# Kernel tuning notes

Measured on AMD Instinct MI355X. Metric: run time of the kernel, lower is better.

## Reference

```python
import jax, jax.numpy as jnp
import numpy as np
from jax import lax

W = 65536  # wavelength batch
L = 64     # number of stacked layers
N_IN = 1.0
N_OUT = 1.45
PURITY = 0.87
CD_SCALE = 32980.0  # mdeg conversion, as in source
LN10 = 2.302585092994046


def setup_inputs() -> dict:
    key = jax.random.key(0)
    ks = jax.random.split(key, 9)
    wl = jnp.linspace(0.4, 0.8, W, dtype=jnp.float32)  # microns, matches wl_range*1e-6 usage
    thickP = jax.random.normal(ks[0], (L,), jnp.float32) * 2.0

    def u(k, lo, hi):
        return lo + (hi - lo) * jax.random.uniform(k, (W, L), jnp.float32)

    return {
        "wl": wl,
        "thickP": thickP,
        "mind": jnp.float32(20.0),   # nm
        "maxd": jnp.float32(300.0),  # nm
        "eps_c_re": u(ks[1], 1.8, 4.5),
        "eps_c_im": u(ks[2], 0.0, 0.08),
        "kappa_c_re": u(ks[3], -5e-3, 5e-3),
        "kappa_c_im": u(ks[4], -5e-3, 5e-3),
        "eps_a_re": u(ks[5], 1.8, 4.5),
        "eps_a_im": u(ks[6], 0.0, 0.08),
        "kappa_a_re": u(ks[7], -5e-3, 5e-3),
        "kappa_a_im": u(ks[8], -5e-3, 5e-3),
    }


def _chain(Ms):
    # Ms: [L, W, 2, 2] complex; sequential layer chain-multiply (TMM recursion)
    eye = jnp.broadcast_to(jnp.eye(2, dtype=Ms.dtype), (Ms.shape[1], 2, 2))

    def step(carry, Ml):
        return jnp.einsum('wij,wjk->wik', carry, Ml), None

    Mt, _ = lax.scan(step, eye, Ms)
    return Mt  # [W, 2, 2]


def _absorbance(eps, kappa, sigma, k0, d):
    # Circular eigenmode TMM for Pasteur (isotropic chiral) layers at normal incidence.
    # eps, kappa: [W, L] complex relative quantities; k0: [W]; d: [L] meters.
    n0 = jnp.sqrt(eps)                       # background index, also wave admittance
    n_sig = n0 + sigma * kappa               # circular eigenmode index n +/- kappa
    delta = k0[:, None] * n_sig * d[None, :]  # [W, L] phase thickness
    c = jnp.cos(delta)
    s = jnp.sin(delta)
    Y = n0
    # characteristic matrix per layer: [[cos d, i sin d / Y], [i Y sin d, cos d]]
    M = jnp.stack([jnp.stack([c, 1j * s / Y], axis=-1),
                   jnp.stack([1j * Y * s, c], axis=-1)], axis=-2)  # [W, L, 2, 2]
    Mt = _chain(jnp.transpose(M, (1, 0, 2, 3)))
    m00, m01 = Mt[:, 0, 0], Mt[:, 0, 1]
    m10, m11 = Mt[:, 1, 0], Mt[:, 1, 1]
    denom = N_IN * (m00 + m01 * N_OUT) + (m10 + m11 * N_OUT)
    t = 2.0 * N_IN / denom
    T = (N_OUT / N_IN) * (jnp.abs(t) ** 2)
    return -jnp.log(T + 1e-12) / LN10  # absorbance per handedness


def _stack_cd_abs(eps_re, eps_im, kap_re, kap_im, k0, d):
    eps = (eps_re + 1j * eps_im).astype(jnp.complex64)
    kap = (kap_re + 1j * kap_im).astype(jnp.complex64)
    A_r = _absorbance(eps, kap, +1.0, k0, d)  # RCP
    A_l = _absorbance(eps, kap, -1.0, k0, d)  # LCP
    return A_l - A_r, 0.5 * (A_l + A_r)


def reference(wl, thickP, mind, maxd, eps_c_re, eps_c_im, kappa_c_re, kappa_c_im,
              eps_a_re, eps_a_im, kappa_a_re, kappa_a_im):
    d = (jax.nn.sigmoid(thickP) * (maxd - mind) + mind) * 1e-9  # [L] meters
    k0 = (2.0 * np.float32(3.1415926)) / (wl * 1e-6)             # [W]
    cd_c, abs_c = _stack_cd_abs(eps_c_re, eps_c_im, kappa_c_re, kappa_c_im, k0, d)
    cd_a, abs_a = _stack_cd_abs(eps_a_re, eps_a_im, kappa_a_re, kappa_a_im, k0, d)
    scale = (2.0 * PURITY - 1.0) * CD_SCALE
    return (cd_c * scale, cd_a * scale, abs_c, abs_a)
```

## Files before the change

kernel.cpp:

```cpp
#include <hip/hip_runtime.h>
#include <math.h>

#define LTOT 64
#define GL   4
#define LPL  (LTOT / GL)

#define INV2PI  0.15915494309189535f
#define LOG2E   1.4426950408889634f
#define LOG10_2 0.30102999566398120f

struct cpx { float r, i; };
struct Mat { cpx e00, e01, e10, e11; };

__device__ __forceinline__ cpx cmul(cpx a, cpx b) {
    return { fmaf(a.r, b.r, -a.i * b.i), fmaf(a.r, b.i, a.i * b.r) };
}
__device__ __forceinline__ cpx cmadd(cpx a, cpx b, cpx c) {
    return { fmaf(a.r, b.r, fmaf(-a.i, b.i, c.r)),
             fmaf(a.r, b.i, fmaf( a.i, b.r, c.i)) };
}
__device__ __forceinline__ Mat mmul(const Mat& A, const Mat& B) {
    Mat C;
    C.e00 = cmadd(A.e01, B.e10, cmul(A.e00, B.e00));
    C.e01 = cmadd(A.e01, B.e11, cmul(A.e00, B.e01));
    C.e10 = cmadd(A.e11, B.e10, cmul(A.e10, B.e00));
    C.e11 = cmadd(A.e11, B.e11, cmul(A.e10, B.e01));
    return C;
}
__device__ __forceinline__ cpx csqrt_pos(cpx z) {
    float m  = __builtin_amdgcn_sqrtf(fmaf(z.r, z.r, z.i * z.i));
    float re = __builtin_amdgcn_sqrtf(0.5f * (m + z.r));
    float im = 0.5f * z.i * __builtin_amdgcn_rcpf(re);
    return { re, im };
}

__device__ __forceinline__ void accum(Mat& P, bool first, float xrev, float y,
                                      cpx n0, float inv_n0sq) {
    float rf = __builtin_amdgcn_fractf(xrev);
    float s_ = __builtin_amdgcn_sinf(rf);
    float c_ = __builtin_amdgcn_cosf(rf);
    float y2 = y * y;
    float chv = fmaf(y2, fmaf(y2, 0.0416666667f, 0.5f), 1.0f);
    float shv = y * fmaf(y2, fmaf(y2, 0.0083333333f, 0.1666666667f), 1.0f);
    cpx cc = { c_ * chv, -s_ * shv };
    cpx ss = { s_ * chv,  c_ * shv };
    cpx qq = { (ss.r * n0.r + ss.i * n0.i) * inv_n0sq,
               (ss.i * n0.r - ss.r * n0.i) * inv_n0sq };
    cpx m01 = { -qq.i, qq.r };
    cpx p   = cmul(n0, ss);
    cpx m10 = { -p.i, p.r };
    if (first) {
        P.e00 = cc; P.e01 = m01; P.e10 = m10; P.e11 = cc;
    } else {
        Mat C;
        C.e00 = cmadd(P.e01, m10, cmul(P.e00, cc));
        C.e01 = cmadd(P.e01, cc,  cmul(P.e00, m01));
        C.e10 = cmadd(P.e11, m10, cmul(P.e10, cc));
        C.e11 = cmadd(P.e11, cc,  cmul(P.e10, m01));
        P = C;
    }
}

__device__ __forceinline__ Mat shfl_mat(const Mat& M, int mask) {
    Mat R;
    R.e00.r = __shfl_xor(M.e00.r, mask); R.e00.i = __shfl_xor(M.e00.i, mask);
    R.e01.r = __shfl_xor(M.e01.r, mask); R.e01.i = __shfl_xor(M.e01.i, mask);
    R.e10.r = __shfl_xor(M.e10.r, mask); R.e10.i = __shfl_xor(M.e10.i, mask);
    R.e11.r = __shfl_xor(M.e11.r, mask); R.e11.i = __shfl_xor(M.e11.i, mask);
    return R;
}

__global__ __launch_bounds__(256) void chiral_kernel(
    const float* __restrict__ wl,  const float* __restrict__ thickP,
    const float* __restrict__ mindp, const float* __restrict__ maxdp,
    const float* __restrict__ ecr, const float* __restrict__ eci,
    const float* __restrict__ kcr, const float* __restrict__ kci,
    const float* __restrict__ ear, const float* __restrict__ eai,
    const float* __restrict__ kar, const float* __restrict__ kai,
    float* __restrict__ out, int W)
{
    int t = blockIdx.x * blockDim.x + threadIdx.x;
    int w = t >> 2;
    int j = t & 3;
    if (w >= W) return;

    float lo = mindp[0], hi = maxdp[0];
    float k0 = 6.2831852e6f * __builtin_amdgcn_rcpf(wl[w]);

    Mat P[4];

    size_t rowbase = (size_t)w * LTOT + (size_t)(LPL * j);

    #pragma unroll
    for (int q4 = 0; q4 < 4; q4++) {
        size_t base = rowbase + 4 * q4;
        float4 tp4   = *reinterpret_cast<const float4*>(thickP + LPL * j + 4 * q4);
        float4 v_ecr = *reinterpret_cast<const float4*>(ecr + base);
        float4 v_eci = *reinterpret_cast<const float4*>(eci + base);
        float4 v_kcr = *reinterpret_cast<const float4*>(kcr + base);
        float4 v_kci = *reinterpret_cast<const float4*>(kci + base);
        float4 v_ear = *reinterpret_cast<const float4*>(ear + base);
        float4 v_eai = *reinterpret_cast<const float4*>(eai + base);
        float4 v_kar = *reinterpret_cast<const float4*>(kar + base);
        float4 v_kai = *reinterpret_cast<const float4*>(kai + base);
        const float* ptp  = reinterpret_cast<const float*>(&tp4);
        const float* pecr = reinterpret_cast<const float*>(&v_ecr);
        const float* peci = reinterpret_cast<const float*>(&v_eci);
        const float* pkcr = reinterpret_cast<const float*>(&v_kcr);
        const float* pkci = reinterpret_cast<const float*>(&v_kci);
        const float* pear = reinterpret_cast<const float*>(&v_ear);
        const float* peai = reinterpret_cast<const float*>(&v_eai);
        const float* pkar = reinterpret_cast<const float*>(&v_kar);
        const float* pkai = reinterpret_cast<const float*>(&v_kai);

        #pragma unroll
        for (int q = 0; q < 4; q++) {
            bool first = (q4 == 0 && q == 0);
            float tr = ptp[q];
            float sg = __builtin_amdgcn_rcpf(1.0f + __builtin_amdgcn_exp2f(-tr * LOG2E));
            float d  = fmaf(sg, (hi - lo), lo) * 1e-9f;
            float kd = k0 * d;

            {
                cpx e  = { pecr[q], peci[q] };
                cpx kp = { pkcr[q], pkci[q] };
                cpx n0 = csqrt_pos(e);
                float inv = __builtin_amdgcn_rcpf(fmaf(n0.r, n0.r, n0.i * n0.i));
                float ar = kd * n0.r, ai = kd * n0.i;
                float br = kd * kp.r, bi = kd * kp.i;
                accum(P[0], first, (ar + br) * INV2PI, ai + bi, n0, inv);
                accum(P[1], first, (ar - br) * INV2PI, ai - bi, n0, inv);
            }
            {
                cpx e  = { pear[q], peai[q] };
                cpx kp = { pkar[q], pkai[q] };
                cpx n0 = csqrt_pos(e);
                float inv = __builtin_amdgcn_rcpf(fmaf(n0.r, n0.r, n0.i * n0.i));
                float ar = kd * n0.r, ai = kd * n0.i;
                float br = kd * kp.r, bi = kd * kp.i;
                accum(P[2], first, (ar + br) * INV2PI, ai + bi, n0, inv);
                accum(P[3], first, (ar - br) * INV2PI, ai - bi, n0, inv);
            }
        }
    }

    #pragma unroll
    for (int m = 1; m < GL; m <<= 1) {
        bool up = (j & m) != 0;
        #pragma unroll
        for (int ch = 0; ch < 4; ch++) {
            Mat O = shfl_mat(P[ch], m);
            Mat Lf, Rt;
            Lf.e00 = up ? O.e00 : P[ch].e00; Lf.e01 = up ? O.e01 : P[ch].e01;
            Lf.e10 = up ? O.e10 : P[ch].e10; Lf.e11 = up ? O.e11 : P[ch].e11;
            Rt.e00 = up ? P[ch].e00 : O.e00; Rt.e01 = up ? P[ch].e01 : O.e01;
            Rt.e10 = up ? P[ch].e10 : O.e10; Rt.e11 = up ? P[ch].e11 : O.e11;
            P[ch] = mmul(Lf, Rt);
        }
    }

    if (j == 0) {
        float A[4];
        #pragma unroll
        for (int ch = 0; ch < 4; ch++) {
            float dr = P[ch].e00.r + 1.45f * P[ch].e01.r + P[ch].e10.r + 1.45f * P[ch].e11.r;
            float di = P[ch].e00.i + 1.45f * P[ch].e01.i + P[ch].e10.i + 1.45f * P[ch].e11.i;
            float den = fmaf(dr, dr, di * di);
            float T = 5.8f * __builtin_amdgcn_rcpf(den);
            A[ch] = -__builtin_amdgcn_logf(T + 1e-12f) * LOG10_2;
        }
        const float SC = (2.0f * 0.87f - 1.0f) * 32980.0f;
        out[0 * W + w] = (A[1] - A[0]) * SC;
        out[1 * W + w] = (A[3] - A[2]) * SC;
        out[2 * W + w] = 0.5f * (A[1] + A[0]);
        out[3 * W + w] = 0.5f * (A[3] + A[2]);
    }
}

extern "C" void kernel_launch(void* const* d_in, const int* in_sizes, int n_in,
                              void* d_out, int out_size, void* d_ws, size_t ws_size,
                              hipStream_t stream) {
    const float* wl     = (const float*)d_in[0];
    const float* thickP = (const float*)d_in[1];
    const float* mind   = (const float*)d_in[2];
    const float* maxd   = (const float*)d_in[3];
    const float* ecr    = (const float*)d_in[4];
    const float* eci    = (const float*)d_in[5];
    const float* kcr    = (const float*)d_in[6];
    const float* kci    = (const float*)d_in[7];
    const float* ear    = (const float*)d_in[8];
    const float* eai    = (const float*)d_in[9];
    const float* kar    = (const float*)d_in[10];
    const float* kai    = (const float*)d_in[11];
    float* out = (float*)d_out;

    int W = in_sizes[0];
    int threads = W * GL;
    int block = 256;
    int grid = (threads + block - 1) / block;
    chiral_kernel<<<grid, block, 0, stream>>>(wl, thickP, mind, maxd,
                                              ecr, eci, kcr, kci,
                                              ear, eai, kar, kai, out, W);
}
```

Before: 188.4 us.

## Split layer chain across 8 lanes, hoist all loads, simplify complex sqrt

Each wavelength's 64-layer chain is now split across 8 lanes of 8 layers each instead of 4 lanes of 16, which adds a third shuffle-reduction stage. All per-thread inputs are loaded up front so more memory requests are in flight. The complex square root now uses rsq and takes |n0|^2 directly from the modulus, removing one rcp and one multiply-add per layer. Launch bounds request 4 blocks per SM, trading more threads and shuffle work for more latency hiding.

```diff
diff --git a/kernel.cpp b/kernel.cpp
--- a/kernel.cpp
+++ b/kernel.cpp
@@ -2,7 +2,7 @@
 #include <math.h>
 
 #define LTOT 64
-#define GL   4
+#define GL   8
 #define LPL  (LTOT / GL)
 
 #define INV2PI  0.15915494309189535f
@@ -27,11 +27,13 @@
     C.e11 = cmadd(A.e11, B.e11, cmul(A.e10, B.e01));
     return C;
 }
-__device__ __forceinline__ cpx csqrt_pos(cpx z) {
-    float m  = __builtin_amdgcn_sqrtf(fmaf(z.r, z.r, z.i * z.i));
-    float re = __builtin_amdgcn_sqrtf(0.5f * (m + z.r));
-    float im = 0.5f * z.i * __builtin_amdgcn_rcpf(re);
-    return { re, im };
+__device__ __forceinline__ void csqrt_inv(cpx z, cpx& n0, float& inv) {
+    float m = __builtin_amdgcn_sqrtf(fmaf(z.r, z.r, z.i * z.i));
+    float x = 0.5f * (m + z.r);
+    float t = __builtin_amdgcn_rsqf(x);
+    n0.r = x * t;
+    n0.i = 0.5f * z.i * t;
+    inv  = __builtin_amdgcn_rcpf(m);
 }
 
 __device__ __forceinline__ void accum(Mat& P, bool first, float xrev, float y,
@@ -70,7 +72,7 @@
     return R;
 }
 
-__global__ __launch_bounds__(256) void chiral_kernel(
+__global__ __launch_bounds__(256, 4) void chiral_kernel(
     const float* __restrict__ wl,  const float* __restrict__ thickP,
     const float* __restrict__ mindp, const float* __restrict__ maxdp,
     const float* __restrict__ ecr, const float* __restrict__ eci,
@@ -80,42 +82,47 @@
     float* __restrict__ out, int W)
 {
     int t = blockIdx.x * blockDim.x + threadIdx.x;
-    int w = t >> 2;
-    int j = t & 3;
+    int w = t >> 3;
+    int j = t & 7;
     if (w >= W) return;
+
+    size_t rowbase = (size_t)w * LTOT + (size_t)(LPL * j);
+
+    float4 Ltp[2], Lecr[2], Leci[2], Lkcr[2], Lkci[2], Lear[2], Leai[2], Lkar[2], Lkai[2];
+    #pragma unroll
+    for (int h = 0; h < 2; h++) {
+        size_t b = rowbase + 4 * h;
+        Ltp[h]  = *reinterpret_cast<const float4*>(thickP + LPL * j + 4 * h);
+        Lecr[h] = *reinterpret_cast<const float4*>(ecr + b);
+        Leci[h] = *reinterpret_cast<const float4*>(eci + b);
+        Lkcr[h] = *reinterpret_cast<const float4*>(kcr + b);
+        Lkci[h] = *reinterpret_cast<const float4*>(kci + b);
+        Lear[h] = *reinterpret_cast<const float4*>(ear + b);
+        Leai[h] = *reinterpret_cast<const float4*>(eai + b);
+        Lkar[h] = *reinterpret_cast<const float4*>(kar + b);
+        Lkai[h] = *reinterpret_cast<const float4*>(kai + b);
+    }
 
     float lo = mindp[0], hi = maxdp[0];
     float k0 = 6.2831852e6f * __builtin_amdgcn_rcpf(wl[w]);
 
     Mat P[4];
 
-    size_t rowbase = (size_t)w * LTOT + (size_t)(LPL * j);
-
     #pragma unroll
-    for (int q4 = 0; q4 < 4; q4++) {
-        size_t base = rowbase + 4 * q4;
-        float4 tp4   = *reinterpret_cast<const float4*>(thickP + LPL * j + 4 * q4);
-        float4 v_ecr = *reinterpret_cast<const float4*>(ecr + base);
-        float4 v_eci = *reinterpret_cast<const float4*>(eci + base);
-        float4 v_kcr = *reinterpret_cast<const float4*>(kcr + base);
-        float4 v_kci = *reinterpret_cast<const float4*>(kci + base);
-        float4 v_ear = *reinterpret_cast<const float4*>(ear + base);
-        float4 v_eai = *reinterpret_cast<const float4*>(eai + base);
-        float4 v_kar = *reinterpret_cast<const float4*>(kar + base);
-        float4 v_kai = *reinterpret_cast<const float4*>(kai + base);
-        const float* ptp  = reinterpret_cast<const float*>(&tp4);
-        const float* pecr = reinterpret_cast<const float*>(&v_ecr);
-        const float* peci = reinterpret_cast<const float*>(&v_eci);
-        const float* pkcr = reinterpret_cast<const float*>(&v_kcr);
-        const float* pkci = reinterpret_cast<const float*>(&v_kci);
-        const float* pear = reinterpret_cast<const float*>(&v_ear);
-        const float* peai = reinterpret_cast<const float*>(&v_eai);
-        const float* pkar = reinterpret_cast<const float*>(&v_kar);
-        const float* pkai = reinterpret_cast<const float*>(&v_kai);
+    for (int h = 0; h < 2; h++) {
+        const float* ptp  = reinterpret_cast<const float*>(&Ltp[h]);
+        const float* pecr = reinterpret_cast<const float*>(&Lecr[h]);
+        const float* peci = reinterpret_cast<const float*>(&Leci[h]);
+        const float* pkcr = reinterpret_cast<const float*>(&Lkcr[h]);
+        const float* pkci = reinterpret_cast<const float*>(&Lkci[h]);
+        const float* pear = reinterpret_cast<const float*>(&Lear[h]);
+        const float* peai = reinterpret_cast<const float*>(&Leai[h]);
+        const float* pkar = reinterpret_cast<const float*>(&Lkar[h]);
+        const float* pkai = reinterpret_cast<const float*>(&Lkai[h]);
 
         #pragma unroll
         for (int q = 0; q < 4; q++) {
-            bool first = (q4 == 0 && q == 0);
+            bool first = (h == 0 && q == 0);
             float tr = ptp[q];
             float sg = __builtin_amdgcn_rcpf(1.0f + __builtin_amdgcn_exp2f(-tr * LOG2E));
             float d  = fmaf(sg, (hi - lo), lo) * 1e-9f;
@@ -124,8 +131,8 @@
             {
                 cpx e  = { pecr[q], peci[q] };
                 cpx kp = { pkcr[q], pkci[q] };
-                cpx n0 = csqrt_pos(e);
-                float inv = __builtin_amdgcn_rcpf(fmaf(n0.r, n0.r, n0.i * n0.i));
+                cpx n0; float inv;
+                csqrt_inv(e, n0, inv);
                 float ar = kd * n0.r, ai = kd * n0.i;
                 float br = kd * kp.r, bi = kd * kp.i;
                 accum(P[0], first, (ar + br) * INV2PI, ai + bi, n0, inv);
@@ -134,8 +141,8 @@
             {
                 cpx e  = { pear[q], peai[q] };
                 cpx kp = { pkar[q], pkai[q] };
-                cpx n0 = csqrt_pos(e);
-                float inv = __builtin_amdgcn_rcpf(fmaf(n0.r, n0.r, n0.i * n0.i));
+                cpx n0; float inv;
+                csqrt_inv(e, n0, inv);
                 float ar = kd * n0.r, ai = kd * n0.i;
                 float br = kd * kp.r, bi = kd * kp.i;
                 accum(P[2], first, (ar + br) * INV2PI, ai + bi, n0, inv);
```

New measurement: 180.1 us. 1.05x faster.
